# Kernel tuning notes

Hardware: AMD Instinct MI355X
Metric: run time of the kernel (lower is better)

## Reference

```python
import jax, jax.numpy as jnp
import numpy as np

MAX_REL_POS = 1024


def rel_to_abs(x):
    """Music Transformer skew: [b,h,l,l] rel logits -> abs-position logits."""
    b, h, l, _ = x.shape
    x = jnp.pad(x, ((0, 0), (0, 0), (0, 0), (1, 0)))  # pad left of last dim
    x = x.reshape(b, h, l + 1, l)
    return x[:, :, 1:l + 1, :l]


def get_rel_embeddings(embed, seq_len):
    m = embed.shape[0]
    pad_len = max(seq_len - m, 0)
    start = max(m - seq_len, 0)
    padded = jnp.pad(embed, ((pad_len, 0), (0, 0)))
    return padded[start:, :]  # [seq_len, d]


def setup_inputs() -> dict:
    key = jax.random.key(0)
    kq, kk, kv, kr = jax.random.split(key, 4)
    B, H, L, D = 2, 8, 2048, 64
    # scale q so logits are O(1) (realistic attention magnitudes)
    q = jax.random.normal(kq, (B, H, L, D), dtype=jnp.float32) * (1.0 / np.sqrt(D))
    k = jax.random.normal(kk, (B, H, L, D), dtype=jnp.float32)
    v = jax.random.normal(kv, (B, H, L, D), dtype=jnp.float32)
    rel_keys_weight = jax.random.normal(kr, (MAX_REL_POS, D), dtype=jnp.float32)
    # causal mask: True = masked (masked_fill semantics)
    mask = jnp.triu(jnp.ones((L, L), dtype=bool), k=1)[None, None]
    return {"q": q, "k": k, "v": v, "rel_keys_weight": rel_keys_weight, "mask": mask}


def reference(q, k, v, rel_keys_weight, mask):
    L = q.shape[2]
    logits = jnp.einsum('bhqd,bhkd->bhqk', q, k)
    rel_keys = get_rel_embeddings(rel_keys_weight, L)          # [L, D]
    rel_logits = jnp.einsum('bhqd,md->bhqm', q, rel_keys)      # [B,H,L,L]
    logits = logits + rel_to_abs(rel_logits)
    logits = jnp.where(mask, -jnp.inf, logits)
    weights = jax.nn.softmax(logits, axis=3)
    output = jnp.matmul(weights, v)
    return (output, weights)
```

## Files before the change

kernel.cpp:

```cpp
#include <hip/hip_runtime.h>
#include <hip/hip_bf16.h>

typedef short bf16x8 __attribute__((ext_vector_type(8)));
typedef float f32x4  __attribute__((ext_vector_type(4)));

#define SEQ  2048
#define HD   64
#define LDT  72
#define TSTR 84
#define PSTR 72
#define OUT0 (16 * SEQ * HD)

__device__ __forceinline__ short f2bf(float x) {
    unsigned u = __float_as_uint(x);
    unsigned r = u + 0x7fffu + ((u >> 16) & 1u);
    return (short)(r >> 16);
}
__device__ __forceinline__ float bf2f(short s) {
    return __uint_as_float(((unsigned)(unsigned short)s) << 16);
}

__device__ __forceinline__ void stage64(const float* __restrict__ src_base,
                                        short* __restrict__ dst, int tid) {
    const int r = tid >> 2, cg = tid & 3;
    const float4* src = (const float4*)(src_base + (size_t)r * HD + cg * 16);
    float f[16];
#pragma unroll
    for (int t = 0; t < 4; ++t) {
        float4 v4 = src[t];
        f[4*t] = v4.x; f[4*t+1] = v4.y; f[4*t+2] = v4.z; f[4*t+3] = v4.w;
    }
    bf16x8 p0, p1;
#pragma unroll
    for (int t = 0; t < 8; ++t) { p0[t] = f2bf(f[t]); p1[t] = f2bf(f[t+8]); }
    *(bf16x8*)&dst[r * LDT + cg * 16]     = p0;
    *(bf16x8*)&dst[r * LDT + cg * 16 + 8] = p1;
}

__device__ __forceinline__ void stageG(const float* __restrict__ eg,
                                       short* __restrict__ Gs, int tid, int i0, int j0) {
    const int dd = tid >> 1, hf = tid & 1;
    const int e = 1086 - i0 + j0 - dd;
    short* dst = &Gs[dd * LDT + hf * 32];
    if (e >= 0 && e < 1024) {
        const float4* src = (const float4*)(eg + (size_t)e * HD + hf * 32);
#pragma unroll
        for (int u = 0; u < 4; ++u) {
            float4 a = src[2*u], b = src[2*u + 1];
            bf16x8 p;
            p[0] = f2bf(a.x); p[1] = f2bf(a.y); p[2] = f2bf(a.z); p[3] = f2bf(a.w);
            p[4] = f2bf(b.x); p[5] = f2bf(b.y); p[6] = f2bf(b.z); p[7] = f2bf(b.w);
            *(bf16x8*)&dst[u * 8] = p;
        }
    } else {
        bf16x8 z = {0,0,0,0,0,0,0,0};
#pragma unroll
        for (int u = 0; u < 4; ++u) *(bf16x8*)&dst[u * 8] = z;
    }
}

__device__ __forceinline__ void compute_sc(const bf16x8* aq, const short* __restrict__ Ks,
                                           const short* __restrict__ Gs, short* __restrict__ Tw,
                                           int wv, int qd, int c, int i0, int j0, f32x4* sc) {
    f32x4 tc[5];
    const f32x4 zz = {0.f, 0.f, 0.f, 0.f};
#pragma unroll
    for (int ct = 0; ct < 4; ++ct) sc[ct] = zz;
#pragma unroll
    for (int dt = 0; dt < 5; ++dt) tc[dt] = zz;
#pragma unroll
    for (int s = 0; s < 2; ++s) {
        bf16x8 a = aq[s];
#pragma unroll
        for (int ct = 0; ct < 4; ++ct) {
            bf16x8 b = *(const bf16x8*)&Ks[(ct * 16 + c) * LDT + s * 32 + qd * 8];
            sc[ct] = __builtin_amdgcn_mfma_f32_16x16x32_bf16(a, b, sc[ct], 0, 0, 0);
        }
#pragma unroll
        for (int dt = 0; dt < 5; ++dt) {
            bf16x8 g = *(const bf16x8*)&Gs[((wv + dt) * 16 + c) * LDT + s * 32 + qd * 8];
            tc[dt] = __builtin_amdgcn_mfma_f32_16x16x32_bf16(a, g, tc[dt], 0, 0, 0);
        }
    }
#pragma unroll
    for (int dt = 0; dt < 5; ++dt)
#pragma unroll
        for (int rg = 0; rg < 4; ++rg)
            Tw[(qd * 4 + rg) * TSTR + dt * 16 + c] = f2bf(tc[dt][rg]);
#pragma unroll
    for (int ct = 0; ct < 4; ++ct)
#pragma unroll
        for (int rg = 0; rg < 4; ++rg) {
            const int rl  = qd * 4 + rg;
            const int ddl = rl + 63 - ct * 16 - c;
            float sval = sc[ct][rg] + bf2f(Tw[rl * TSTR + ddl]);
            const int ig = i0 + wv * 16 + rl;
            const int jg = j0 + ct * 16 + c;
            sc[ct][rg] = (jg <= ig) ? sval : -3.0e38f;
        }
}

__global__ __launch_bounds__(256, 2)
void relattn(const float* __restrict__ qg, const float* __restrict__ kg,
             const float* __restrict__ vg, const float* __restrict__ eg,
             float* __restrict__ outp)
{
    __shared__ short Qs[64 * LDT];
    __shared__ short Ks[64 * LDT];
    __shared__ short Vt[64 * LDT];
    __shared__ short Gs[128 * LDT];
    __shared__ short TP[4 * 16 * TSTR];

    const int tid  = threadIdx.x;
    const int wv   = tid >> 6;
    const int lane = tid & 63;
    const int qd   = lane >> 4;
    const int c    = lane & 15;

    const int bh = blockIdx.x & 15;
    const int qt = 31 - (blockIdx.x >> 4);
    const int i0 = qt * 64;

    float* Wg = outp + OUT0;

    {
        const int z0v = (qt + 1) * 16;
        for (int r = 0; r < 64; ++r) {
            float4* dst = (float4*)(Wg + ((size_t)(bh * SEQ + i0 + r)) * SEQ);
            for (int jv = z0v + tid; jv < SEQ / 4; jv += 256)
                dst[jv] = make_float4(0.f, 0.f, 0.f, 0.f);
        }
    }

    stage64(qg + ((size_t)(bh * SEQ + i0)) * HD, Qs, tid);
    __syncthreads();
    bf16x8 aq[2];
#pragma unroll
    for (int s = 0; s < 2; ++s)
        aq[s] = *(const bf16x8*)&Qs[(wv * 16 + c) * LDT + s * 32 + qd * 8];

    short* Tw = &TP[wv * 16 * TSTR];

    float mrun[4], lrun[4];
#pragma unroll
    for (int rg = 0; rg < 4; ++rg) { mrun[rg] = -3.0e38f; lrun[rg] = 0.f; }

    for (int kt = 0; kt <= qt; ++kt) {
        const int j0 = kt * 64;
        __syncthreads();
        stage64(kg + ((size_t)(bh * SEQ + j0)) * HD, Ks, tid);
        stageG(eg, Gs, tid, i0, j0);
        __syncthreads();

        f32x4 sc[4];
        compute_sc(aq, Ks, Gs, Tw, wv, qd, c, i0, j0, sc);

#pragma unroll
        for (int rg = 0; rg < 4; ++rg) {
            float mx = fmaxf(fmaxf(sc[0][rg], sc[1][rg]), fmaxf(sc[2][rg], sc[3][rg]));
            mx = fmaxf(mx, __shfl_xor(mx, 1));
            mx = fmaxf(mx, __shfl_xor(mx, 2));
            mx = fmaxf(mx, __shfl_xor(mx, 4));
            mx = fmaxf(mx, __shfl_xor(mx, 8));
            const float mnew = fmaxf(mrun[rg], mx);
            float ss = __expf(sc[0][rg] - mnew) + __expf(sc[1][rg] - mnew)
                     + __expf(sc[2][rg] - mnew) + __expf(sc[3][rg] - mnew);
            ss += __shfl_xor(ss, 1);
            ss += __shfl_xor(ss, 2);
            ss += __shfl_xor(ss, 4);
            ss += __shfl_xor(ss, 8);
            lrun[rg] = lrun[rg] * __expf(mrun[rg] - mnew) + ss;
            mrun[rg] = mnew;
        }
    }

    float linv[4];
#pragma unroll
    for (int rg = 0; rg < 4; ++rg) linv[rg] = 1.0f / lrun[rg];

    f32x4 ob[4];
    {
        const f32x4 zz = {0.f, 0.f, 0.f, 0.f};
#pragma unroll
        for (int dt = 0; dt < 4; ++dt) ob[dt] = zz;
    }

    for (int kt = 0; kt <= qt; ++kt) {
        const int j0 = kt * 64;
        __syncthreads();
        stage64(kg + ((size_t)(bh * SEQ + j0)) * HD, Ks, tid);
        stageG(eg, Gs, tid, i0, j0);
        {
            const int r = tid >> 2, cg = tid & 3;
            const float4* src = (const float4*)(vg + ((size_t)(bh * SEQ + j0 + r)) * HD + cg * 16);
            float f[16];
#pragma unroll
            for (int t = 0; t < 4; ++t) {
                float4 v4 = src[t];
                f[4*t] = v4.x; f[4*t+1] = v4.y; f[4*t+2] = v4.z; f[4*t+3] = v4.w;
            }
#pragma unroll
            for (int t = 0; t < 16; ++t) Vt[(cg * 16 + t) * LDT + r] = f2bf(f[t]);
        }
        __syncthreads();

        f32x4 sc[4];
        compute_sc(aq, Ks, Gs, Tw, wv, qd, c, i0, j0, sc);

#pragma unroll
        for (int rg = 0; rg < 4; ++rg) {
            const int rl = qd * 4 + rg;
            const int ig = i0 + wv * 16 + rl;
            float* wrow = Wg + ((size_t)(bh * SEQ + ig)) * SEQ + j0;
#pragma unroll
            for (int ct = 0; ct < 4; ++ct) {
                const float w = __expf(sc[ct][rg] - mrun[rg]) * linv[rg];
                wrow[ct * 16 + c] = w;
                Tw[rl * PSTR + ct * 16 + c] = f2bf(w);
            }
        }

#pragma unroll
        for (int s = 0; s < 2; ++s) {
            bf16x8 ap = *(const bf16x8*)&Tw[c * PSTR + s * 32 + qd * 8];
#pragma unroll
            for (int dt = 0; dt < 4; ++dt) {
                bf16x8 bv = *(const bf16x8*)&Vt[(dt * 16 + c) * LDT + s * 32 + qd * 8];
                ob[dt] = __builtin_amdgcn_mfma_f32_16x16x32_bf16(ap, bv, ob[dt], 0, 0, 0);
            }
        }
    }

#pragma unroll
    for (int dt = 0; dt < 4; ++dt)
#pragma unroll
        for (int rg = 0; rg < 4; ++rg) {
            const int ig = i0 + wv * 16 + qd * 4 + rg;
            outp[((size_t)(bh * SEQ + ig)) * HD + dt * 16 + c] = ob[dt][rg];
        }
}

extern "C" void kernel_launch(void* const* d_in, const int* in_sizes, int n_in,
                              void* d_out, int out_size, void* d_ws, size_t ws_size,
                              hipStream_t stream) {
    const float* q = (const float*)d_in[0];
    const float* k = (const float*)d_in[1];
    const float* v = (const float*)d_in[2];
    const float* e = (const float*)d_in[3];
    float* out = (float*)d_out;
    hipLaunchKernelGGL(relattn, dim3(512), dim3(256), 0, stream, q, k, v, e, out);
}
```

Before: 453.4 us.

## Double-buffer K/V tiles, ring-buffer rel embeddings, shuffle-based skew

Switches K and V to double-buffered shared memory and prefetches the next tile into registers while the current tile is being computed, so each loop iteration needs only one barrier. The relative-embedding tile becomes a 192-row ring buffer that loads only 64 new rows per step instead of 128. The skew gather now uses cross-lane shuffles rather than an LDS round trip through bf16. The causal mask is applied only on the diagonal tile, and query tiles are interleaved to balance work across blocks. The cost is higher register and LDS use, which may lower occupancy.

```diff
diff --git a/kernel.cpp b/kernel.cpp
--- a/kernel.cpp
+++ b/kernel.cpp
@@ -4,70 +4,115 @@
 typedef short bf16x8 __attribute__((ext_vector_type(8)));
 typedef float f32x4  __attribute__((ext_vector_type(4)));
 
-#define SEQ  2048
-#define HD   64
-#define LDT  72
-#define TSTR 84
-#define PSTR 72
-#define OUT0 (16 * SEQ * HD)
+#define SEQ   2048
+#define HD    64
+#define LDT   72
+#define TSTR  84
+#define GROWS 192
+#define OUT0  (16 * SEQ * HD)
 
 __device__ __forceinline__ short f2bf(float x) {
     unsigned u = __float_as_uint(x);
     unsigned r = u + 0x7fffu + ((u >> 16) & 1u);
     return (short)(r >> 16);
 }
-__device__ __forceinline__ float bf2f(short s) {
-    return __uint_as_float(((unsigned)(unsigned short)s) << 16);
-}
-
-__device__ __forceinline__ void stage64(const float* __restrict__ src_base,
-                                        short* __restrict__ dst, int tid) {
+
+struct F16 { float4 a[4]; };
+
+__device__ __forceinline__ void cvt8(const float4& x, const float4& y, bf16x8& p) {
+    p[0] = f2bf(x.x); p[1] = f2bf(x.y); p[2] = f2bf(x.z); p[3] = f2bf(x.w);
+    p[4] = f2bf(y.x); p[5] = f2bf(y.y); p[6] = f2bf(y.z); p[7] = f2bf(y.w);
+}
+
+__device__ __forceinline__ void issue64(const float* __restrict__ base, int tid, F16& f) {
     const int r = tid >> 2, cg = tid & 3;
-    const float4* src = (const float4*)(src_base + (size_t)r * HD + cg * 16);
-    float f[16];
-#pragma unroll
-    for (int t = 0; t < 4; ++t) {
-        float4 v4 = src[t];
-        f[4*t] = v4.x; f[4*t+1] = v4.y; f[4*t+2] = v4.z; f[4*t+3] = v4.w;
-    }
+    const float4* src = (const float4*)(base + (size_t)r * HD + cg * 16);
+#pragma unroll
+    for (int t = 0; t < 4; ++t) f.a[t] = src[t];
+}
+__device__ __forceinline__ void write64(short* __restrict__ dst, int tid, const F16& f) {
+    const int r = tid >> 2, cg = tid & 3;
     bf16x8 p0, p1;
-#pragma unroll
-    for (int t = 0; t < 8; ++t) { p0[t] = f2bf(f[t]); p1[t] = f2bf(f[t+8]); }
+    cvt8(f.a[0], f.a[1], p0);
+    cvt8(f.a[2], f.a[3], p1);
     *(bf16x8*)&dst[r * LDT + cg * 16]     = p0;
     *(bf16x8*)&dst[r * LDT + cg * 16 + 8] = p1;
 }
 
-__device__ __forceinline__ void stageG(const float* __restrict__ eg,
-                                       short* __restrict__ Gs, int tid, int i0, int j0) {
+__device__ __forceinline__ void issueG(const float* __restrict__ eg, int tid, int etop, F16& f) {
+    const int r = tid >> 2, cg = tid & 3;
+    const int e = etop - r;
+    if (e >= 0 && e < 1024) {
+        const float4* src = (const float4*)(eg + (size_t)e * HD + cg * 16);
+#pragma unroll
+        for (int t = 0; t < 4; ++t) f.a[t] = src[t];
+    } else {
+        const float4 z = make_float4(0.f, 0.f, 0.f, 0.f);
+#pragma unroll
+        for (int t = 0; t < 4; ++t) f.a[t] = z;
+    }
+}
+__device__ __forceinline__ void writeG(short* __restrict__ Gr, int tid, int sbn, const F16& f) {
+    const int r = tid >> 2, cg = tid & 3;
+    int sl = r + sbn; if (sl >= GROWS) sl -= GROWS;
+    bf16x8 p0, p1;
+    cvt8(f.a[0], f.a[1], p0);
+    cvt8(f.a[2], f.a[3], p1);
+    *(bf16x8*)&Gr[sl * LDT + cg * 16]     = p0;
+    *(bf16x8*)&Gr[sl * LDT + cg * 16 + 8] = p1;
+}
+
+__device__ __forceinline__ void stageG_full(const float* __restrict__ eg, short* __restrict__ Gr,
+                                            int tid, int i0) {
     const int dd = tid >> 1, hf = tid & 1;
-    const int e = 1086 - i0 + j0 - dd;
-    short* dst = &Gs[dd * LDT + hf * 32];
+    const int e = 1086 - i0 - dd;
+    int sl = dd + 128; if (sl >= GROWS) sl -= GROWS;
+    short* dst = &Gr[sl * LDT + hf * 32];
     if (e >= 0 && e < 1024) {
         const float4* src = (const float4*)(eg + (size_t)e * HD + hf * 32);
 #pragma unroll
         for (int u = 0; u < 4; ++u) {
-            float4 a = src[2*u], b = src[2*u + 1];
-            bf16x8 p;
-            p[0] = f2bf(a.x); p[1] = f2bf(a.y); p[2] = f2bf(a.z); p[3] = f2bf(a.w);
-            p[4] = f2bf(b.x); p[5] = f2bf(b.y); p[6] = f2bf(b.z); p[7] = f2bf(b.w);
+            bf16x8 p; cvt8(src[2 * u], src[2 * u + 1], p);
             *(bf16x8*)&dst[u * 8] = p;
         }
     } else {
-        bf16x8 z = {0,0,0,0,0,0,0,0};
+        bf16x8 z = {0, 0, 0, 0, 0, 0, 0, 0};
 #pragma unroll
         for (int u = 0; u < 4; ++u) *(bf16x8*)&dst[u * 8] = z;
     }
 }
 
+__device__ __forceinline__ void issueV(const float* __restrict__ vbase, int tid, F16& f) {
+    const int r = tid & 63, cg = tid >> 6;
+    const float4* src = (const float4*)(vbase + (size_t)r * HD + cg * 16);
+#pragma unroll
+    for (int t = 0; t < 4; ++t) f.a[t] = src[t];
+}
+__device__ __forceinline__ void writeV(short* __restrict__ Vt, int tid, const F16& f) {
+    const int r = tid & 63, cg = tid >> 6;
+    const float* ff = (const float*)&f.a[0];
+#pragma unroll
+    for (int t = 0; t < 16; ++t)
+        Vt[(cg * 16 + t) * LDT + r] = f2bf(ff[t]);
+}
+
 __device__ __forceinline__ void compute_sc(const bf16x8* aq, const short* __restrict__ Ks,
-                                           const short* __restrict__ Gs, short* __restrict__ Tw,
-                                           int wv, int qd, int c, int i0, int j0, f32x4* sc) {
+                                           const short* __restrict__ Gr, int sb,
+                                           int wv, int qd, int c, int lane,
+                                           f32x4* sc, bool diag) {
     f32x4 tc[5];
     const f32x4 zz = {0.f, 0.f, 0.f, 0.f};
 #pragma unroll
     for (int ct = 0; ct < 4; ++ct) sc[ct] = zz;
 #pragma unroll
     for (int dt = 0; dt < 5; ++dt) tc[dt] = zz;
+    int sl[5];
+#pragma unroll
+    for (int dt = 0; dt < 5; ++dt) {
+        int s0 = (wv + dt) * 16 + sb + c;
+        if (s0 >= GROWS) s0 -= GROWS;
+        sl[dt] = s0 * LDT;
+    }
 #pragma unroll
     for (int s = 0; s < 2; ++s) {
         bf16x8 a = aq[s];
@@ -78,26 +123,25 @@
         }
 #pragma unroll
         for (int dt = 0; dt < 5; ++dt) {
-            bf16x8 g = *(const bf16x8*)&Gs[((wv + dt) * 16 + c) * LDT + s * 32 + qd * 8];
+            bf16x8 g = *(const bf16x8*)&Gr[sl[dt] + s * 32 + qd * 8];
             tc[dt] = __builtin_amdgcn_mfma_f32_16x16x32_bf16(a, g, tc[dt], 0, 0, 0);
         }
     }
 #pragma unroll
-    for (int dt = 0; dt < 5; ++dt)
-#pragma unroll
-        for (int rg = 0; rg < 4; ++rg)
-            Tw[(qd * 4 + rg) * TSTR + dt * 16 + c] = f2bf(tc[dt][rg]);
-#pragma unroll
-    for (int ct = 0; ct < 4; ++ct)
-#pragma unroll
-        for (int rg = 0; rg < 4; ++rg) {
-            const int rl  = qd * 4 + rg;
-            const int ddl = rl + 63 - ct * 16 - c;
-            float sval = sc[ct][rg] + bf2f(Tw[rl * TSTR + ddl]);
-            const int ig = i0 + wv * 16 + rl;
-            const int jg = j0 + ct * 16 + c;
-            sc[ct][rg] = (jg <= ig) ? sval : -3.0e38f;
-        }
+    for (int rg = 0; rg < 4; ++rg) {
+        const int rl  = qd * 4 + rg;
+        const int cp  = (rl + 63 - c) & 15;
+        const int src = (lane & 48) | cp;
+        const bool hi = (rl + 63 - cp) >= 64;
+#pragma unroll
+        for (int ct = 0; ct < 4; ++ct) {
+            float vs = hi ? tc[4 - ct][rg] : tc[3 - ct][rg];
+            float tr = __shfl(vs, src, 64);
+            float sval = sc[ct][rg] + tr;
+            if (diag && (ct * 16 + c > wv * 16 + rl)) sval = -3.0e38f;
+            sc[ct][rg] = sval;
+        }
+    }
 }
 
 __global__ __launch_bounds__(256, 2)
@@ -105,11 +149,10 @@
              const float* __restrict__ vg, const float* __restrict__ eg,
              float* __restrict__ outp)
 {
-    __shared__ short Qs[64 * LDT];
-    __shared__ short Ks[64 * LDT];
-    __shared__ short Vt[64 * LDT];
-    __shared__ short Gs[128 * LDT];
-    __shared__ short TP[4 * 16 * TSTR];
+    __shared__ short Ks2[2][64 * LDT];
+    __shared__ short Gr[GROWS * LDT];
+    __shared__ short Vt2[2][64 * LDT];
+    __shared__ short Ps[4 * 16 * TSTR];
 
     const int tid  = threadIdx.x;
     const int wv   = tid >> 6;
@@ -118,7 +161,8 @@
     const int c    = lane & 15;
 
     const int bh = blockIdx.x & 15;
-    const int qt = 31 - (blockIdx.x >> 4);
+    const int u  = blockIdx.x >> 4;
+    const int qt = (u < 16) ? u : 47 - u;
     const int i0 = qt * 64;
 
     float* Wg = outp + OUT0;
@@ -132,28 +176,39 @@
         }
     }
 
-    stage64(qg + ((size_t)(bh * SEQ + i0)) * HD, Qs, tid);
+    {
+        F16 fq; issue64(qg + ((size_t)(bh * SEQ + i0)) * HD, tid, fq);
+        write64(Ks2[0], tid, fq);
+    }
     __syncthreads();
     bf16x8 aq[2];
 #pragma unroll
     for (int s = 0; s < 2; ++s)
-        aq[s] = *(const bf16x8*)&Qs[(wv * 16 + c) * LDT + s * 32 + qd * 8];
-
-    short* Tw = &TP[wv * 16 * TSTR];
+        aq[s] = *(const bf16x8*)&Ks2[0][(wv * 16 + c) * LDT + s * 32 + qd * 8];
+    __syncthreads();
 
     float mrun[4], lrun[4];
 #pragma unroll
     for (int rg = 0; rg < 4; ++rg) { mrun[rg] = -3.0e38f; lrun[rg] = 0.f; }
 
+    {
+        F16 fk; issue64(kg + ((size_t)(bh * SEQ)) * HD, tid, fk);
+        write64(Ks2[0], tid, fk);
+        stageG_full(eg, Gr, tid, i0);
+    }
+    __syncthreads();
+    int sb = 128;
     for (int kt = 0; kt <= qt; ++kt) {
-        const int j0 = kt * 64;
-        __syncthreads();
-        stage64(kg + ((size_t)(bh * SEQ + j0)) * HD, Ks, tid);
-        stageG(eg, Gs, tid, i0, j0);
-        __syncthreads();
-
+        const int cur = kt & 1;
+        const bool pf = kt < qt;
+        const int sbn = (sb >= 64) ? sb - 64 : sb + 128;
+        F16 fk, fg;
+        if (pf) {
+            issue64(kg + ((size_t)(bh * SEQ + (kt + 1) * 64)) * HD, tid, fk);
+            issueG(eg, tid, 1086 - i0 + 64 * (kt + 1), fg);
+        }
         f32x4 sc[4];
-        compute_sc(aq, Ks, Gs, Tw, wv, qd, c, i0, j0, sc);
+        compute_sc(aq, Ks2[cur], Gr, sb, wv, qd, c, lane, sc, kt == qt);
 
 #pragma unroll
         for (int rg = 0; rg < 4; ++rg) {
@@ -172,6 +227,12 @@
             lrun[rg] = lrun[rg] * __expf(mrun[rg] - mnew) + ss;
             mrun[rg] = mnew;
         }
+        if (pf) {
+            write64(Ks2[cur ^ 1], tid, fk);
+            writeG(Gr, tid, sbn, fg);
+        }
+        sb = sbn;
+        __syncthreads();
     }
 
     float linv[4];
@@ -185,27 +246,29 @@
         for (int dt = 0; dt < 4; ++dt) ob[dt] = zz;
     }
 
+    {
+        F16 fk; issue64(kg + ((size_t)(bh * SEQ)) * HD, tid, fk);
+        write64(Ks2[0], tid, fk);
+        stageG_full(eg, Gr, tid, i0);
+        F16 fv; issueV(vg + ((size_t)(bh * SEQ)) * HD, tid, fv);
+        writeV(Vt2[0], tid, fv);
+    }
+    __syncthreads();
+    sb = 128;
+    short* Pw = &Ps[wv * 16 * TSTR];
     for (int kt = 0; kt <= qt; ++kt) {
+        const int cur = kt & 1;
+        const bool pf = kt < qt;
+        const int sbn = (sb >= 64) ? sb - 64 : sb + 128;
         const int j0 = kt * 64;
-        __syncthreads();
-        stage64(kg + ((size_t)(bh * SEQ + j0)) * HD, Ks, tid);
-        stageG(eg, Gs, tid, i0, j0);
-        {
-            const int r = tid >> 2, cg = tid & 3;
-            const float4* src = (const float4*)(vg + ((size_t)(bh * SEQ + j0 + r)) * HD + cg * 16);
-            float f[16];
-#pragma unroll
-            for (int t = 0; t < 4; ++t) {
-                float4 v4 = src[t];
-                f[4*t] = v4.x; f[4*t+1] = v4.y; f[4*t+2] = v4.z; f[4*t+3] = v4.w;
-            }
-#pragma unroll
-            for (int t = 0; t < 16; ++t) Vt[(cg * 16 + t) * LDT + r] = f2bf(f[t]);
-        }
-        __syncthreads();
-
+        F16 fk, fg, fv;
+        if (pf) {
+            issue64(kg + ((size_t)(bh * SEQ + j0 + 64)) * HD, tid, fk);
+            issueG(eg, tid, 1086 - i0 + j0 + 64, fg);
+            issueV(vg + ((size_t)(bh * SEQ + j0 + 64)) * HD, tid, fv);
+        }
         f32x4 sc[4];
-        compute_sc(aq, Ks, Gs, Tw, wv, qd, c, i0, j0, sc);
+        compute_sc(aq, Ks2[cur], Gr, sb, wv, qd, c, lane, sc, kt == qt);
 
 #pragma unroll
         for (int rg = 0; rg < 4; ++rg) {
@@ -216,19 +279,26 @@
             for (int ct = 0; ct < 4; ++ct) {
                 const float w = __expf(sc[ct][rg] - mrun[rg]) * linv[rg];
                 wrow[ct * 16 + c] = w;
-                Tw[rl * PSTR + ct * 16 + c] = f2bf(w);
+                Pw[rl * TSTR + ct * 16 + c] = f2bf(w);
             }
         }
 
 #pragma unroll
         for (int s = 0; s < 2; ++s) {
-            bf16x8 ap = *(const bf16x8*)&Tw[c * PSTR + s * 32 + qd * 8];
+            bf16x8 ap = *(const bf16x8*)&Pw[c * TSTR + s * 32 + qd * 8];
 #pragma unroll
             for (int dt = 0; dt < 4; ++dt) {
-                bf16x8 bv = *(const bf16x8*)&Vt[(dt * 16 + c) * LDT + s * 32 + qd * 8];
+                bf16x8 bv = *(const bf16x8*)&Vt2[cur][(dt * 16 + c) * LDT + s * 32 + qd * 8];
                 ob[dt] = __builtin_amdgcn_mfma_f32_16x16x32_bf16(ap, bv, ob[dt], 0, 0, 0);
             }
         }
+        if (pf) {
+            write64(Ks2[cur ^ 1], tid, fk);
+            writeG(Gr, tid, sbn, fg);
+            writeV(Vt2[cur ^ 1], tid, fv);
+        }
+        sb = sbn;
+        __syncthreads();
     }
 
 #pragma unroll
```

New measurement: 404.2 us. 1.12x faster.
